# Optimization experiments

Hardware: AMD Instinct MI355X
Metric: run time of the kernel (lower is better)

## Reference

```python
import jax, jax.numpy as jnp
import numpy as np
import math

N, D, E, M, MODS = 16384, 1024, 5, 64, 5
K = 1  # top-k for sparse router


def setup_inputs() -> dict:
    key = jax.random.key(0)
    ks = jax.random.split(key, 24)
    rn = lambda k, shape, s=1.0: jax.random.normal(k, shape, dtype=jnp.float32) * s
    inp = {
        'x': rn(ks[0], (N, D)),
        'spectrogram': rn(ks[1], (N, D)),
        'waveform': rn(ks[2], (N, D)),
        'pitch': rn(ks[3], (N, D)),
        'envelope': rn(ks[4], (N, D)),
        'phase': rn(ks[5], (N, D)),
        # routers (torch Linear: y = x @ W.T + b, W is [out,in]); init std=0.01
        'Wsoft': rn(ks[6], (E, D), 0.01), 'bsoft': jnp.zeros((E,), jnp.float32),
        'Wsparse': rn(ks[7], (E, D), 0.01), 'bsparse': jnp.zeros((E,), jnp.float32),
        # memory (plain randn, not re-initialized)
        'm_key': rn(ks[8], (M, D)), 'm_val': rn(ks[9], (M, E)),
        # experts: Linear(D,D) -> SiLU -> Linear(D,D), stacked over E
        'W1': rn(ks[10], (E, D, D), 0.01), 'b1': jnp.zeros((E, D), jnp.float32),
        'W2': rn(ks[11], (E, D, D), 0.01), 'b2': jnp.zeros((E, D), jnp.float32),
        # fusion gates: Linear(D,1) + sigmoid, one per modality
        'Wg': rn(ks[12], (MODS, D), 0.01), 'bg': jnp.zeros((MODS,), jnp.float32),
        # fusion projection: Linear(D*MODS, D)
        'Wf': rn(ks[13], (D, D * MODS), 0.01), 'bf': jnp.zeros((D,), jnp.float32),
    }
    return inp


def reference(x, spectrogram, waveform, pitch, envelope, phase,
              Wsoft, bsoft, Wsparse, bsparse, m_key, m_val,
              W1, b1, W2, b2, Wg, bg, Wf, bf):
    alpha_moe = jnp.float32(0.5)
    alpha_fusion = jnp.float32(0.5)

    # soft router: softmax(Linear)
    soft_w = jax.nn.softmax(x @ Wsoft.T + bsoft, axis=-1)          # [N,E]

    # sparse router: top-k + softmax, scattered back to [N,E]
    logits = x @ Wsparse.T + bsparse                               # [N,E]
    top_vals, top_idx = jax.lax.top_k(logits, K)                   # [N,K]
    sparse_gates = jax.nn.softmax(top_vals, axis=-1)               # [N,K]
    one_hot = jax.nn.one_hot(top_idx, E, dtype=logits.dtype)       # [N,K,E]
    sparse_w = jnp.sum(one_hot * sparse_gates[..., None], axis=1)  # [N,E]

    # memory-augmented gating
    attn = jax.nn.softmax((x @ m_key.T) / math.sqrt(D), axis=-1)   # [N,M]
    memory_w = jax.nn.softmax(attn @ m_val, axis=-1)               # [N,E]

    mixed_w = alpha_moe * sparse_w + (1 - alpha_moe) * soft_w
    final_w = (mixed_w + memory_w) / 2                             # [N,E]

    # dense all-expert MLP: [N,E,D]
    h = jax.nn.silu(jnp.einsum('nd,eod->neo', x, W1) + b1)
    expert_out = jnp.einsum('ned,eod->neo', h, W2) + b2
    moe_output = jnp.einsum('neo,ne->no', expert_out, final_w)     # [N,D]

    # gated multimodal fusion
    features = [spectrogram, waveform, pitch, envelope, phase]
    gates = jax.nn.sigmoid(x @ Wg.T + bg)                          # [N,MODS]
    scaled = [gates[:, q:q + 1] * features[q] for q in range(MODS)]
    fused = jnp.concatenate(scaled, axis=-1) @ Wf.T + bf           # [N,D]

    return alpha_fusion * fused + (1 - alpha_fusion) * moe_output
```

## Files before the change

kernel.cpp:

```cpp
#include <hip/hip_runtime.h>
#include <stdint.h>

typedef __bf16 bf16x8 __attribute__((ext_vector_type(8)));
typedef float f32x4 __attribute__((ext_vector_type(4)));
typedef unsigned short u16;
typedef u16 ushort8 __attribute__((ext_vector_type(8)));

__device__ __forceinline__ u16 f2bf(float f) {
    uint32_t u = __builtin_bit_cast(uint32_t, f);
    u += 0x7FFFu + ((u >> 16) & 1u);
    return (u16)(u >> 16);
}

__device__ __forceinline__ void gload16(const void* g, void* l) {
    __builtin_amdgcn_global_load_lds(
        reinterpret_cast<const __attribute__((address_space(1))) void*>(reinterpret_cast<uintptr_t>(g)),
        reinterpret_cast<__attribute__((address_space(3))) void*>(reinterpret_cast<uintptr_t>(l)),
        16, 0, 0);
}

#define BAR() asm volatile("s_barrier" ::: "memory")

template <int MODE>
__global__ __launch_bounds__(512, 2)
void gemm256(const u16* __restrict__ A, int lda,
             const u16* __restrict__ B, int ldb, int K,
             void* __restrict__ Cout, int ldc,
             const float* __restrict__ bias, const float* __restrict__ fw05)
{
    __shared__ __align__(16) u16 As[2 * 256 * 64];
    __shared__ __align__(16) u16 Bs[2 * 256 * 64];

    const int t    = threadIdx.x;
    const int lane = t & 63;
    const int wave = t >> 6;
    const int l16  = lane & 15;
    const int lhi  = lane >> 4;
    const int wm   = wave >> 2;
    const int wn   = wave & 3;

    const size_t rowBase = (size_t)blockIdx.y * 256;
    const int    colBase = blockIdx.x * 256;
    const int    NT      = K >> 6;

    const int rl0 = t >> 3;
    const int ko0 = (t & 7) * 8;
    const int kos = ((t & 7) ^ (rl0 & 7)) * 8;

    const u16* aRow = A + (rowBase + rl0) * (size_t)lda + kos;
    const u16* bRow = B + (size_t)(colBase + rl0) * ldb + kos;
    u16* asW = As + rl0 * 64 + ko0;
    u16* bsW = Bs + rl0 * 64 + ko0;

#define STA(bufo, e, r0, r1)                                                     \
    do {                                                                         \
        gload16(aRow + (size_t)(r0) * lda + (e), asW + (bufo) + (r0) * 64);      \
        gload16(aRow + (size_t)(r1) * lda + (e), asW + (bufo) + (r1) * 64);      \
    } while (0)
#define STB(bufo, e, b0)                                                         \
    do {                                                                         \
        gload16(bRow + (size_t)(b0) * ldb + (e), bsW + (bufo) + (b0) * 64);      \
        gload16(bRow + (size_t)((b0) + 64) * ldb + (e),                          \
                bsW + (bufo) + ((b0) + 64) * 64);                                \
    } while (0)

    const int sw = l16 & 7;
    const u16* aRd0 = As + (wm * 128 + l16) * 64 + ((lhi ^ sw) * 8);
    const u16* aRd1 = As + (wm * 128 + l16) * 64 + (((lhi + 4) ^ sw) * 8);
    const u16* bRd0 = Bs + (wn * 64 + l16) * 64 + ((lhi ^ sw) * 8);
    const u16* bRd1 = Bs + (wn * 64 + l16) * 64 + (((lhi + 4) ^ sw) * 8);

    f32x4 acc[8][4];
#pragma unroll
    for (int i = 0; i < 8; i++)
#pragma unroll
        for (int j = 0; j < 4; j++)
            acc[i][j] = (f32x4){0.f, 0.f, 0.f, 0.f};

    STA(0, 0, 0, 128);
    STA(0, 0, 64, 192);
    STB(0, 0, 0);
    STB(0, 0, 128);
    const int e1p = (NT > 1) ? 64 : 0;
    STB(16384, e1p, 0);
    STB(16384, e1p, 128);
    STA(16384, e1p, 0, 128);
    asm volatile("s_waitcnt vmcnt(6)" ::: "memory");
    BAR();

    bf16x8 bfr[4][2];
    for (int tt = 0; tt < NT; ++tt) {
        const int c  = (tt & 1) << 14;
        const int cn = c ^ 16384;
        const int e1 = ((tt + 1 < NT) ? tt + 1 : NT - 1) << 6;
        const int e2 = ((tt + 2 < NT) ? tt + 2 : NT - 1) << 6;

#pragma unroll
        for (int q = 0; q < 4; ++q) {
            bf16x8 af[2][2];
#pragma unroll
            for (int s = 0; s < 2; ++s) {
                af[s][0] = *(const bf16x8*)(aRd0 + c + (2 * q + s) * 16 * 64);
                af[s][1] = *(const bf16x8*)(aRd1 + c + (2 * q + s) * 16 * 64);
            }
            if (q == 0) {
#pragma unroll
                for (int ni = 0; ni < 4; ++ni) {
                    bfr[ni][0] = *(const bf16x8*)(bRd0 + c + ni * 16 * 64);
                    bfr[ni][1] = *(const bf16x8*)(bRd1 + c + ni * 16 * 64);
                }
                STA(cn, e1, 64, 192);
            } else if (q == 1) {
                STB(c, e2, 0);
            } else if (q == 2) {
                STB(c, e2, 128);
            } else {
                STA(c, e2, 0, 128);
            }
            BAR();
            __builtin_amdgcn_s_setprio(1);
#pragma unroll
            for (int s = 0; s < 2; ++s)
#pragma unroll
                for (int ni = 0; ni < 4; ++ni)
#pragma unroll
                    for (int kk = 0; kk < 2; ++kk)
                        acc[2 * q + s][ni] = __builtin_amdgcn_mfma_f32_16x16x32_bf16(
                            af[s][kk], bfr[ni][kk], acc[2 * q + s][ni], 0, 0, 0);
            __builtin_amdgcn_s_setprio(0);
            if (q == 3) asm volatile("s_waitcnt vmcnt(6)" ::: "memory");
            BAR();
        }
    }

    const int orow = wm * 128 + lhi * 4;
    const int ocol = colBase + wn * 64 + l16;

    if constexpr (MODE == 0) {
        u16* C = (u16*)Cout;
#pragma unroll
        for (int mi = 0; mi < 8; mi++) {
#pragma unroll
            for (int j = 0; j < 4; j++) {
                size_t r = rowBase + orow + mi * 16 + j;
#pragma unroll
                for (int ni = 0; ni < 4; ni++) {
                    int cc = ocol + ni * 16;
                    float v = acc[mi][ni][j] + bias[cc];
                    float s = v / (1.f + __expf(-v));
                    C[r * (size_t)ldc + cc] = f2bf(fw05[r * 5 + (cc >> 10)] * s);
                }
            }
        }
    } else {
        float* C = (float*)Cout;
#pragma unroll
        for (int mi = 0; mi < 8; mi++) {
#pragma unroll
            for (int j = 0; j < 4; j++) {
                size_t r = rowBase + orow + mi * 16 + j;
#pragma unroll
                for (int ni = 0; ni < 4; ni++) {
                    size_t idx = r * (size_t)ldc + (ocol + ni * 16);
                    if constexpr (MODE == 1) C[idx] = acc[mi][ni][j];
                    else                     C[idx] += acc[mi][ni][j];
                }
            }
        }
    }
#undef STA
#undef STB
}

__global__ __launch_bounds__(256)
void router_kernel(const float* __restrict__ x,
                   const float* __restrict__ Wsoft, const float* __restrict__ Wsparse,
                   const float* __restrict__ m_key, const float* __restrict__ Wg,
                   float* __restrict__ logits)
{
    __shared__ float Xs[128][66];
    __shared__ float Ws[80][132];

    const int t    = threadIdx.x;
    const int lane = t & 63;
    const int wave = t >> 6;
    const int row0 = blockIdx.x * 64;

    float acc[20];
#pragma unroll
    for (int c = 0; c < 20; c++) acc[c] = 0.f;

    for (int k0 = 0; k0 < 1024; k0 += 128) {
#pragma unroll
        for (int i = 0; i < 8; i++) {
            int f4 = i * 256 + t;
            int r  = f4 >> 5;
            int kk = (f4 & 31) * 4;
            f32x4 v = *(const f32x4*)(x + (size_t)(row0 + r) * 1024 + k0 + kk);
            Xs[kk + 0][r] = v[0]; Xs[kk + 1][r] = v[1];
            Xs[kk + 2][r] = v[2]; Xs[kk + 3][r] = v[3];
        }
#pragma unroll
        for (int i = 0; i < 10; i++) {
            int f4 = i * 256 + t;
            int j  = f4 >> 5;
            int kk = (f4 & 31) * 4;
            const float* src;
            if      (j < 5)  src = Wsoft   + (size_t)j * 1024;
            else if (j < 10) src = Wsparse + (size_t)(j - 5) * 1024;
            else if (j < 74) src = m_key   + (size_t)(j - 10) * 1024;
            else             src = Wg      + (size_t)(j - 74) * 1024;
            *(f32x4*)&Ws[j][kk] = *(const f32x4*)(src + k0 + kk);
        }
        __syncthreads();

        for (int k4 = 0; k4 < 32; k4++) {
            float x0 = Xs[k4 * 4 + 0][lane];
            float x1 = Xs[k4 * 4 + 1][lane];
            float x2 = Xs[k4 * 4 + 2][lane];
            float x3 = Xs[k4 * 4 + 3][lane];
#pragma unroll
            for (int c = 0; c < 20; c++) {
                f32x4 w = *(const f32x4*)&Ws[wave * 20 + c][k4 * 4];
                acc[c] += x0 * w[0] + x1 * w[1] + x2 * w[2] + x3 * w[3];
            }
        }
        __syncthreads();
    }

    float* dst = logits + (size_t)(row0 + lane) * 80 + wave * 20;
#pragma unroll
    for (int c = 0; c < 20; c++) dst[c] = acc[c];
}

__global__ __launch_bounds__(256)
void finalize_kernel(const float* __restrict__ logits, const float* __restrict__ m_val,
                     const float* __restrict__ bsoft, const float* __restrict__ bsparse,
                     const float* __restrict__ bg,
                     float* __restrict__ fw05, float* __restrict__ g05, int NC)
{
    __shared__ float mv[320];
    for (int i = threadIdx.x; i < 320; i += 256) mv[i] = m_val[i];
    __syncthreads();

    int idx = blockIdx.x * 256 + threadIdx.x;
    if (idx >= NC) return;
    const float* L = logits + (size_t)idx * 80;

    float sl[5];
#pragma unroll
    for (int e = 0; e < 5; e++) sl[e] = L[e] + bsoft[e];
    float sm = sl[0];
#pragma unroll
    for (int e = 1; e < 5; e++) sm = fmaxf(sm, sl[e]);
    float ssum = 0.f, sw[5];
#pragma unroll
    for (int e = 0; e < 5; e++) { sw[e] = __expf(sl[e] - sm); ssum += sw[e]; }
    float sinv = 1.f / ssum;

    int am = 0; float bv = L[5] + bsparse[0];
#pragma unroll
    for (int e = 1; e < 5; e++) {
        float v = L[5 + e] + bsparse[e];
        if (v > bv) { bv = v; am = e; }
    }

    float amax = -1e30f;
    for (int m = 0; m < 64; m++) amax = fmaxf(amax, L[10 + m] * 0.03125f);
    float asum = 0.f, mw[5] = {0.f, 0.f, 0.f, 0.f, 0.f};
    for (int m = 0; m < 64; m++) {
        float a = __expf(L[10 + m] * 0.03125f - amax);
        asum += a;
#pragma unroll
        for (int e = 0; e < 5; e++) mw[e] += a * mv[m * 5 + e];
    }
    float ainv = 1.f / asum;
#pragma unroll
    for (int e = 0; e < 5; e++) mw[e] *= ainv;
    float mm = mw[0];
#pragma unroll
    for (int e = 1; e < 5; e++) mm = fmaxf(mm, mw[e]);
    float msum = 0.f, me[5];
#pragma unroll
    for (int e = 0; e < 5; e++) { me[e] = __expf(mw[e] - mm); msum += me[e]; }
    float minv = 1.f / msum;

#pragma unroll
    for (int e = 0; e < 5; e++)
        fw05[(size_t)idx * 5 + e] =
            0.125f * ((e == am) ? 1.f : 0.f) + 0.125f * sw[e] * sinv + 0.25f * me[e] * minv;
#pragma unroll
    for (int q = 0; q < 5; q++)
        g05[(size_t)idx * 5 + q] = 0.5f / (1.f + __expf(-(L[74 + q] + bg[q])));
}

__global__ __launch_bounds__(256)
void cast_bf16_kernel(const float* __restrict__ src, u16* __restrict__ dst, size_t n)
{
    size_t i = ((size_t)blockIdx.x * 256 + threadIdx.x) * 8;
    if (i >= n) return;
    f32x4 a = *(const f32x4*)(src + i);
    f32x4 b = *(const f32x4*)(src + i + 4);
    ushort8 o;
    o[0] = f2bf(a[0]); o[1] = f2bf(a[1]); o[2] = f2bf(a[2]); o[3] = f2bf(a[3]);
    o[4] = f2bf(b[0]); o[5] = f2bf(b[1]); o[6] = f2bf(b[2]); o[7] = f2bf(b[3]);
    *(ushort8*)(dst + i) = o;
}

__global__ __launch_bounds__(256)
void prep_w2cat(const float* __restrict__ W2, const float* __restrict__ b2,
                u16* __restrict__ out)
{
    size_t tid = (size_t)blockIdx.x * 256 + threadIdx.x;
    int o  = (int)(tid / 648);
    int c0 = (int)(tid % 648) * 8;
    ushort8 v;
    if (c0 + 8 <= 5120) {
        int e = c0 >> 10, d = c0 & 1023;
        const float* s = W2 + ((size_t)e * 1024 + o) * 1024 + d;
        f32x4 a = *(const f32x4*)s;
        f32x4 b = *(const f32x4*)(s + 4);
        v[0] = f2bf(a[0]); v[1] = f2bf(a[1]); v[2] = f2bf(a[2]); v[3] = f2bf(a[3]);
        v[4] = f2bf(b[0]); v[5] = f2bf(b[1]); v[6] = f2bf(b[2]); v[7] = f2bf(b[3]);
    } else {
#pragma unroll
        for (int jj = 0; jj < 8; jj++) {
            int c = c0 + jj;
            float f = (c >= 5120 && c < 5125) ? b2[(size_t)(c - 5120) * 1024 + o] : 0.f;
            v[jj] = f2bf(f);
        }
    }
    *(ushort8*)(out + (size_t)o * 5184 + c0) = v;
}

__global__ __launch_bounds__(256)
void prep_wfcat(const float* __restrict__ Wf, const float* __restrict__ bfias,
                u16* __restrict__ out)
{
    size_t tid = (size_t)blockIdx.x * 256 + threadIdx.x;
    int o  = (int)(tid / 648);
    int c0 = (int)(tid % 648) * 8;
    ushort8 v;
    if (c0 + 8 <= 5120) {
        const float* s = Wf + (size_t)o * 5120 + c0;
        f32x4 a = *(const f32x4*)s;
        f32x4 b = *(const f32x4*)(s + 4);
        v[0] = f2bf(a[0]); v[1] = f2bf(a[1]); v[2] = f2bf(a[2]); v[3] = f2bf(a[3]);
        v[4] = f2bf(b[0]); v[5] = f2bf(b[1]); v[6] = f2bf(b[2]); v[7] = f2bf(b[3]);
    } else {
#pragma unroll
        for (int jj = 0; jj < 8; jj++) {
            int c = c0 + jj;
            v[jj] = f2bf((c == 5120) ? bfias[o] : 0.f);
        }
    }
    *(ushort8*)(out + (size_t)o * 5184 + c0) = v;
}

__global__ __launch_bounds__(256)
void build_afused(const float* __restrict__ f0, const float* __restrict__ f1,
                  const float* __restrict__ f2, const float* __restrict__ f3,
                  const float* __restrict__ f4,
                  const float* __restrict__ g05, u16* __restrict__ Abuf)
{
    size_t tid = (size_t)blockIdx.x * 256 + threadIdx.x;
    size_t r  = tid / 640;
    int   c0  = (int)(tid % 640) * 8;
    int   q   = c0 >> 10;
    int   d   = c0 & 1023;
    const float* fq = (q == 0) ? f0 : (q == 1) ? f1 : (q == 2) ? f2 : (q == 3) ? f3 : f4;
    float g = g05[r * 5 + q];
    f32x4 a = *(const f32x4*)(fq + r * 1024 + d);
    f32x4 b = *(const f32x4*)(fq + r * 1024 + d + 4);
    ushort8 v;
    v[0] = f2bf(g * a[0]); v[1] = f2bf(g * a[1]); v[2] = f2bf(g * a[2]); v[3] = f2bf(g * a[3]);
    v[4] = f2bf(g * b[0]); v[5] = f2bf(g * b[1]); v[6] = f2bf(g * b[2]); v[7] = f2bf(g * b[3]);
    *(ushort8*)(Abuf + r * 5184 + c0) = v;
}

__global__ __launch_bounds__(256)
void fill_tail(const float* __restrict__ fw05, u16* __restrict__ Abuf, int NC, int mode)
{
    int r = blockIdx.x * 256 + threadIdx.x;
    if (r >= NC) return;
    u16* dst = Abuf + (size_t)r * 5184 + 5120;
    if (mode == 0) {
#pragma unroll
        for (int e = 0; e < 5; e++) dst[e] = f2bf(fw05[(size_t)r * 5 + e]);
        for (int j = 5; j < 64; j++) dst[j] = 0;
    } else {
        dst[0] = f2bf(0.5f);
        for (int j = 1; j < 64; j++) dst[j] = 0;
    }
}

extern "C" void kernel_launch(void* const* d_in, const int* in_sizes, int n_in,
                              void* d_out, int out_size, void* d_ws, size_t ws_size,
                              hipStream_t stream)
{
    (void)in_sizes; (void)n_in; (void)out_size;

    const float* x      = (const float*)d_in[0];
    const float* spect  = (const float*)d_in[1];
    const float* wavef  = (const float*)d_in[2];
    const float* pitch  = (const float*)d_in[3];
    const float* envel  = (const float*)d_in[4];
    const float* phase  = (const float*)d_in[5];
    const float* Wsoft  = (const float*)d_in[6];
    const float* bsoft  = (const float*)d_in[7];
    const float* Wsparse= (const float*)d_in[8];
    const float* bsparse= (const float*)d_in[9];
    const float* m_key  = (const float*)d_in[10];
    const float* m_val  = (const float*)d_in[11];
    const float* W1     = (const float*)d_in[12];
    const float* b1     = (const float*)d_in[13];
    const float* W2     = (const float*)d_in[14];
    const float* b2     = (const float*)d_in[15];
    const float* Wg     = (const float*)d_in[16];
    const float* bg     = (const float*)d_in[17];
    const float* Wf     = (const float*)d_in[18];
    const float* bfias  = (const float*)d_in[19];
    float* out = (float*)d_out;

    const int N = 16384;

    size_t fixed = (size_t)5 * 1024 * 1024 * 2 + 2 * (size_t)1024 * 5184 * 2;
    int NC = 16384;
    while (NC > 256 && fixed + (size_t)NC * 12776 > ws_size) NC >>= 1;

    char* p = (char*)d_ws;
    u16* W1bf  = (u16*)p; p += (size_t)5 * 1024 * 1024 * 2;
    u16* W2cat = (u16*)p; p += (size_t)1024 * 5184 * 2;
    u16* Wfcat = (u16*)p; p += (size_t)1024 * 5184 * 2;
    u16* Xbf   = (u16*)p; p += (size_t)NC * 1024 * 2;
    u16* Abuf  = (u16*)p; p += (size_t)NC * 5184 * 2;
    float* logits = (float*)p; p += (size_t)NC * 80 * 4;
    float* fw05   = (float*)p; p += (size_t)NC * 5 * 4;
    float* g05    = (float*)p; p += (size_t)NC * 5 * 4;

    cast_bf16_kernel<<<2560, 256, 0, stream>>>(W1, W1bf, (size_t)5 * 1024 * 1024);
    prep_w2cat<<<2592, 256, 0, stream>>>(W2, b2, W2cat);
    prep_wfcat<<<2592, 256, 0, stream>>>(Wf, bfias, Wfcat);

    for (int n0 = 0; n0 < N; n0 += NC) {
        const float* xc = x + (size_t)n0 * 1024;

        router_kernel<<<NC / 64, 256, 0, stream>>>(xc, Wsoft, Wsparse, m_key, Wg, logits);
        finalize_kernel<<<(NC + 255) / 256, 256, 0, stream>>>(logits, m_val, bsoft, bsparse, bg,
                                                              fw05, g05, NC);
        cast_bf16_kernel<<<NC / 2, 256, 0, stream>>>(xc, Xbf, (size_t)NC * 1024);

        gemm256<0><<<dim3(20, NC / 256), 512, 0, stream>>>(
            Xbf, 1024, W1bf, 1024, 1024, Abuf, 5184, b1, fw05);
        fill_tail<<<(NC + 255) / 256, 256, 0, stream>>>(fw05, Abuf, NC, 0);

        gemm256<1><<<dim3(4, NC / 256), 512, 0, stream>>>(
            Abuf, 5184, W2cat, 5184, 5184, out + (size_t)n0 * 1024, 1024, nullptr, nullptr);

        build_afused<<<(unsigned)((size_t)NC * 640 / 256), 256, 0, stream>>>(
            spect + (size_t)n0 * 1024, wavef + (size_t)n0 * 1024,
            pitch + (size_t)n0 * 1024, envel + (size_t)n0 * 1024,
            phase + (size_t)n0 * 1024, g05, Abuf);
        fill_tail<<<(NC + 255) / 256, 256, 0, stream>>>(fw05, Abuf, NC, 1);

        gemm256<2><<<dim3(4, NC / 256), 512, 0, stream>>>(
            Abuf, 5184, Wfcat, 5184, 5184, out + (size_t)n0 * 1024, 1024, nullptr, nullptr);
    }
}
```

Measured before the change: 747.0 us.

## Merge MoE and fusion GEMMs into one K-concatenated GEMM, fuse prep kernels

Concatenates the expert-down GEMM and the fusion-projection GEMM along K into a single GEMM of K=10368 that writes the output directly, removing the read-modify-write second pass. The gated feature scaling is folded into the first GEMM's epilogue, the x bf16 cast into the router kernel, and the bias/tail columns into finalize, so build_afused, fill_tail and cast kernels are gone. It also adds a grouped block-index swizzle for L2 locality. The cost is a larger activation buffer (possibly smaller chunks on a tight workspace) and a heavier, less balanced GEMM epilogue in the first GEMM.

```diff
diff --git a/kernel.cpp b/kernel.cpp
--- a/kernel.cpp
+++ b/kernel.cpp
@@ -5,6 +5,7 @@
 typedef float f32x4 __attribute__((ext_vector_type(4)));
 typedef unsigned short u16;
 typedef u16 ushort8 __attribute__((ext_vector_type(8)));
+typedef u16 ushort4v __attribute__((ext_vector_type(4)));
 
 __device__ __forceinline__ u16 f2bf(float f) {
     uint32_t u = __builtin_bit_cast(uint32_t, f);
@@ -26,7 +27,11 @@
 void gemm256(const u16* __restrict__ A, int lda,
              const u16* __restrict__ B, int ldb, int K,
              void* __restrict__ Cout, int ldc,
-             const float* __restrict__ bias, const float* __restrict__ fw05)
+             const float* __restrict__ bias, const float* __restrict__ fw05,
+             const float* __restrict__ g05,
+             const float* __restrict__ f0, const float* __restrict__ f1,
+             const float* __restrict__ f2, const float* __restrict__ f3,
+             const float* __restrict__ f4)
 {
     __shared__ __align__(16) u16 As[2 * 256 * 64];
     __shared__ __align__(16) u16 Bs[2 * 256 * 64];
@@ -39,8 +44,15 @@
     const int wm   = wave >> 2;
     const int wn   = wave & 3;
 
-    const size_t rowBase = (size_t)blockIdx.y * 256;
-    const int    colBase = blockIdx.x * 256;
+    const int gx  = gridDim.x;
+    const int nwg = gx * gridDim.y;
+    int id  = blockIdx.y * gx + blockIdx.x;
+    int swz = (nwg & 7) ? id : ((id & 7) * (nwg >> 3) + (id >> 3));
+    const int bx = swz % gx;
+    const int by = swz / gx;
+
+    const size_t rowBase = (size_t)by * 256;
+    const int    colBase = bx * 256;
     const int    NT      = K >> 6;
 
     const int rl0 = t >> 3;
@@ -138,18 +150,42 @@
 
     if constexpr (MODE == 0) {
         u16* C = (u16*)Cout;
+        const int eidx = colBase >> 10;
 #pragma unroll
         for (int mi = 0; mi < 8; mi++) {
 #pragma unroll
             for (int j = 0; j < 4; j++) {
                 size_t r = rowBase + orow + mi * 16 + j;
+                float w = fw05[r * 5 + eidx];
 #pragma unroll
                 for (int ni = 0; ni < 4; ni++) {
                     int cc = ocol + ni * 16;
                     float v = acc[mi][ni][j] + bias[cc];
                     float s = v / (1.f + __expf(-v));
-                    C[r * (size_t)ldc + cc] = f2bf(fw05[r * 5 + (cc >> 10)] * s);
+                    C[r * (size_t)ldc + cc] = f2bf(w * s);
                 }
+            }
+        }
+        {
+            const float* fq = (eidx == 0) ? f0 : (eidx == 1) ? f1
+                             : (eidx == 2) ? f2 : (eidx == 3) ? f3 : f4;
+            const int dbase = colBase & 1023;
+            const int r2  = t >> 1;
+            const int cb0 = (t & 1) * 128;
+            const size_t r = rowBase + r2;
+            const float g = g05[r * 5 + eidx];
+            const float* fr = fq + r * 1024 + dbase + cb0;
+            u16* dst = C + r * (size_t)ldc + 5184 + colBase + cb0;
+#pragma unroll
+            for (int i = 0; i < 16; ++i) {
+                f32x4 a = *(const f32x4*)(fr + i * 8);
+                f32x4 b = *(const f32x4*)(fr + i * 8 + 4);
+                ushort8 v;
+                v[0] = f2bf(g * a[0]); v[1] = f2bf(g * a[1]);
+                v[2] = f2bf(g * a[2]); v[3] = f2bf(g * a[3]);
+                v[4] = f2bf(g * b[0]); v[5] = f2bf(g * b[1]);
+                v[6] = f2bf(g * b[2]); v[7] = f2bf(g * b[3]);
+                *(ushort8*)(dst + i * 8) = v;
             }
         }
     } else {
@@ -162,8 +198,7 @@
 #pragma unroll
                 for (int ni = 0; ni < 4; ni++) {
                     size_t idx = r * (size_t)ldc + (ocol + ni * 16);
-                    if constexpr (MODE == 1) C[idx] = acc[mi][ni][j];
-                    else                     C[idx] += acc[mi][ni][j];
+                    C[idx] = acc[mi][ni][j];
                 }
             }
         }
@@ -176,7 +211,7 @@
 void router_kernel(const float* __restrict__ x,
                    const float* __restrict__ Wsoft, const float* __restrict__ Wsparse,
                    const float* __restrict__ m_key, const float* __restrict__ Wg,
-                   float* __restrict__ logits)
+                   float* __restrict__ logits, u16* __restrict__ Xbf)
 {
     __shared__ float Xs[128][66];
     __shared__ float Ws[80][132];
@@ -199,6 +234,10 @@
             f32x4 v = *(const f32x4*)(x + (size_t)(row0 + r) * 1024 + k0 + kk);
             Xs[kk + 0][r] = v[0]; Xs[kk + 1][r] = v[1];
             Xs[kk + 2][r] = v[2]; Xs[kk + 3][r] = v[3];
+            ushort4v o4;
+            o4[0] = f2bf(v[0]); o4[1] = f2bf(v[1]);
+            o4[2] = f2bf(v[2]); o4[3] = f2bf(v[3]);
+            *(ushort4v*)(Xbf + (size_t)(row0 + r) * 1024 + k0 + kk) = o4;
         }
 #pragma unroll
         for (int i = 0; i < 10; i++) {
@@ -237,7 +276,8 @@
 void finalize_kernel(const float* __restrict__ logits, const float* __restrict__ m_val,
                      const float* __restrict__ bsoft, const float* __restrict__ bsparse,
                      const float* __restrict__ bg,
-                     float* __restrict__ fw05, float* __restrict__ g05, int NC)
+                     float* __restrict__ fw05, float* __restrict__ g05,
+                     u16* __restrict__ Abuf, int NC)
 {
     __shared__ float mv[320];
     for (int i = threadIdx.x; i < 320; i += 256) mv[i] = m_val[i];
@@ -285,13 +325,21 @@
     for (int e = 0; e < 5; e++) { me[e] = __expf(mw[e] - mm); msum += me[e]; }
     float minv = 1.f / msum;
 
-#pragma unroll
-    for (int e = 0; e < 5; e++)
-        fw05[(size_t)idx * 5 + e] =
-            0.125f * ((e == am) ? 1.f : 0.f) + 0.125f * sw[e] * sinv + 0.25f * me[e] * minv;
+    u16* ta = Abuf + (size_t)idx * 10368;
+#pragma unroll
+    for (int e = 0; e < 5; e++) {
+        float fv = 0.125f * ((e == am) ? 1.f : 0.f) + 0.125f * sw[e] * sinv
+                 + 0.25f * me[e] * minv;
+        fw05[(size_t)idx * 5 + e] = fv;
+        ta[5120 + e] = f2bf(fv);
+    }
 #pragma unroll
     for (int q = 0; q < 5; q++)
         g05[(size_t)idx * 5 + q] = 0.5f / (1.f + __expf(-(L[74 + q] + bg[q])));
+
+    for (int j = 5125; j < 5184; j++) ta[j] = 0;
+    ta[10304] = f2bf(0.5f);
+    for (int j = 10305; j < 10368; j++) ta[j] = 0;
 }
 
 __global__ __launch_bounds__(256)
@@ -308,12 +356,13 @@
 }
 
 __global__ __launch_bounds__(256)
-void prep_w2cat(const float* __restrict__ W2, const float* __restrict__ b2,
-                u16* __restrict__ out)
+void prep_wcat(const float* __restrict__ W2, const float* __restrict__ b2,
+               const float* __restrict__ Wf, const float* __restrict__ bfias,
+               u16* __restrict__ out)
 {
     size_t tid = (size_t)blockIdx.x * 256 + threadIdx.x;
-    int o  = (int)(tid / 648);
-    int c0 = (int)(tid % 648) * 8;
+    int o  = (int)(tid / 1296);
+    int c0 = (int)(tid % 1296) * 8;
     ushort8 v;
     if (c0 + 8 <= 5120) {
         int e = c0 >> 10, d = c0 & 1023;
@@ -322,76 +371,30 @@
         f32x4 b = *(const f32x4*)(s + 4);
         v[0] = f2bf(a[0]); v[1] = f2bf(a[1]); v[2] = f2bf(a[2]); v[3] = f2bf(a[3]);
         v[4] = f2bf(b[0]); v[5] = f2bf(b[1]); v[6] = f2bf(b[2]); v[7] = f2bf(b[3]);
-    } else {
+    } else if (c0 < 5184) {
 #pragma unroll
         for (int jj = 0; jj < 8; jj++) {
             int c = c0 + jj;
             float f = (c >= 5120 && c < 5125) ? b2[(size_t)(c - 5120) * 1024 + o] : 0.f;
             v[jj] = f2bf(f);
         }
-    }
-    *(ushort8*)(out + (size_t)o * 5184 + c0) = v;
-}
-
-__global__ __launch_bounds__(256)
-void prep_wfcat(const float* __restrict__ Wf, const float* __restrict__ bfias,
-                u16* __restrict__ out)
-{
-    size_t tid = (size_t)blockIdx.x * 256 + threadIdx.x;
-    int o  = (int)(tid / 648);
-    int c0 = (int)(tid % 648) * 8;
-    ushort8 v;
-    if (c0 + 8 <= 5120) {
-        const float* s = Wf + (size_t)o * 5120 + c0;
-        f32x4 a = *(const f32x4*)s;
-        f32x4 b = *(const f32x4*)(s + 4);
-        v[0] = f2bf(a[0]); v[1] = f2bf(a[1]); v[2] = f2bf(a[2]); v[3] = f2bf(a[3]);
-        v[4] = f2bf(b[0]); v[5] = f2bf(b[1]); v[6] = f2bf(b[2]); v[7] = f2bf(b[3]);
     } else {
-#pragma unroll
-        for (int jj = 0; jj < 8; jj++) {
-            int c = c0 + jj;
-            v[jj] = f2bf((c == 5120) ? bfias[o] : 0.f);
-        }
-    }
-    *(ushort8*)(out + (size_t)o * 5184 + c0) = v;
-}
-
-__global__ __launch_bounds__(256)
-void build_afused(const float* __restrict__ f0, const float* __restrict__ f1,
-                  const float* __restrict__ f2, const float* __restrict__ f3,
-                  const float* __restrict__ f4,
-                  const float* __restrict__ g05, u16* __restrict__ Abuf)
-{
-    size_t tid = (size_t)blockIdx.x * 256 + threadIdx.x;
-    size_t r  = tid / 640;
-    int   c0  = (int)(tid % 640) * 8;
-    int   q   = c0 >> 10;
-    int   d   = c0 & 1023;
-    const float* fq = (q == 0) ? f0 : (q == 1) ? f1 : (q == 2) ? f2 : (q == 3) ? f3 : f4;
-    float g = g05[r * 5 + q];
-    f32x4 a = *(const f32x4*)(fq + r * 1024 + d);
-    f32x4 b = *(const f32x4*)(fq + r * 1024 + d + 4);
-    ushort8 v;
-    v[0] = f2bf(g * a[0]); v[1] = f2bf(g * a[1]); v[2] = f2bf(g * a[2]); v[3] = f2bf(g * a[3]);
-    v[4] = f2bf(g * b[0]); v[5] = f2bf(g * b[1]); v[6] = f2bf(g * b[2]); v[7] = f2bf(g * b[3]);
-    *(ushort8*)(Abuf + r * 5184 + c0) = v;
-}
-
-__global__ __launch_bounds__(256)
-void fill_tail(const float* __restrict__ fw05, u16* __restrict__ Abuf, int NC, int mode)
-{
-    int r = blockIdx.x * 256 + threadIdx.x;
-    if (r >= NC) return;
-    u16* dst = Abuf + (size_t)r * 5184 + 5120;
-    if (mode == 0) {
-#pragma unroll
-        for (int e = 0; e < 5; e++) dst[e] = f2bf(fw05[(size_t)r * 5 + e]);
-        for (int j = 5; j < 64; j++) dst[j] = 0;
-    } else {
-        dst[0] = f2bf(0.5f);
-        for (int j = 1; j < 64; j++) dst[j] = 0;
-    }
+        int c2 = c0 - 5184;
+        if (c2 + 8 <= 5120) {
+            const float* s = Wf + (size_t)o * 5120 + c2;
+            f32x4 a = *(const f32x4*)s;
+            f32x4 b = *(const f32x4*)(s + 4);
+            v[0] = f2bf(a[0]); v[1] = f2bf(a[1]); v[2] = f2bf(a[2]); v[3] = f2bf(a[3]);
+            v[4] = f2bf(b[0]); v[5] = f2bf(b[1]); v[6] = f2bf(b[2]); v[7] = f2bf(b[3]);
+        } else {
+#pragma unroll
+            for (int jj = 0; jj < 8; jj++) {
+                int cj = c2 + jj;
+                v[jj] = f2bf((cj == 5120) ? bfias[o] : 0.f);
+            }
+        }
+    }
+    *(ushort8*)(out + (size_t)o * 10368 + c0) = v;
 }
 
 extern "C" void kernel_launch(void* const* d_in, const int* in_sizes, int n_in,
@@ -424,46 +427,36 @@
 
     const int N = 16384;
 
-    size_t fixed = (size_t)5 * 1024 * 1024 * 2 + 2 * (size_t)1024 * 5184 * 2;
+    size_t fixed = (size_t)5 * 1024 * 1024 * 2 + (size_t)1024 * 10368 * 2;
     int NC = 16384;
-    while (NC > 256 && fixed + (size_t)NC * 12776 > ws_size) NC >>= 1;
+    while (NC > 256 && fixed + (size_t)NC * 23144 > ws_size) NC >>= 1;
 
     char* p = (char*)d_ws;
-    u16* W1bf  = (u16*)p; p += (size_t)5 * 1024 * 1024 * 2;
-    u16* W2cat = (u16*)p; p += (size_t)1024 * 5184 * 2;
-    u16* Wfcat = (u16*)p; p += (size_t)1024 * 5184 * 2;
-    u16* Xbf   = (u16*)p; p += (size_t)NC * 1024 * 2;
-    u16* Abuf  = (u16*)p; p += (size_t)NC * 5184 * 2;
+    u16* W1bf = (u16*)p; p += (size_t)5 * 1024 * 1024 * 2;
+    u16* Wcat = (u16*)p; p += (size_t)1024 * 10368 * 2;
+    u16* Xbf  = (u16*)p; p += (size_t)NC * 1024 * 2;
+    u16* Abuf = (u16*)p; p += (size_t)NC * 10368 * 2;
     float* logits = (float*)p; p += (size_t)NC * 80 * 4;
     float* fw05   = (float*)p; p += (size_t)NC * 5 * 4;
     float* g05    = (float*)p; p += (size_t)NC * 5 * 4;
 
     cast_bf16_kernel<<<2560, 256, 0, stream>>>(W1, W1bf, (size_t)5 * 1024 * 1024);
-    prep_w2cat<<<2592, 256, 0, stream>>>(W2, b2, W2cat);
-    prep_wfcat<<<2592, 256, 0, stream>>>(Wf, bfias, Wfcat);
+    prep_wcat<<<5184, 256, 0, stream>>>(W2, b2, Wf, bfias, Wcat);
 
     for (int n0 = 0; n0 < N; n0 += NC) {
-        const float* xc = x + (size_t)n0 * 1024;
-
-        router_kernel<<<NC / 64, 256, 0, stream>>>(xc, Wsoft, Wsparse, m_key, Wg, logits);
-        finalize_kernel<<<(NC + 255) / 256, 256, 0, stream>>>(logits, m_val, bsoft, bsparse, bg,
-                                                              fw05, g05, NC);
-        cast_bf16_kernel<<<NC / 2, 256, 0, stream>>>(xc, Xbf, (size_t)NC * 1024);
+        const size_t off = (size_t)n0 * 1024;
+
+        router_kernel<<<NC / 64, 256, 0, stream>>>(x + off, Wsoft, Wsparse, m_key, Wg,
+                                                   logits, Xbf);
+        finalize_kernel<<<(NC + 255) / 256, 256, 0, stream>>>(
+            logits, m_val, bsoft, bsparse, bg, fw05, g05, Abuf, NC);
 
         gemm256<0><<<dim3(20, NC / 256), 512, 0, stream>>>(
-            Xbf, 1024, W1bf, 1024, 1024, Abuf, 5184, b1, fw05);
-        fill_tail<<<(NC + 255) / 256, 256, 0, stream>>>(fw05, Abuf, NC, 0);
+            Xbf, 1024, W1bf, 1024, 1024, Abuf, 10368, b1, fw05, g05,
+            spect + off, wavef + off, pitch + off, envel + off, phase + off);
 
         gemm256<1><<<dim3(4, NC / 256), 512, 0, stream>>>(
-            Abuf, 5184, W2cat, 5184, 5184, out + (size_t)n0 * 1024, 1024, nullptr, nullptr);
-
-        build_afused<<<(unsigned)((size_t)NC * 640 / 256), 256, 0, stream>>>(
-            spect + (size_t)n0 * 1024, wavef + (size_t)n0 * 1024,
-            pitch + (size_t)n0 * 1024, envel + (size_t)n0 * 1024,
-            phase + (size_t)n0 * 1024, g05, Abuf);
-        fill_tail<<<(NC + 255) / 256, 256, 0, stream>>>(fw05, Abuf, NC, 1);
-
-        gemm256<2><<<dim3(4, NC / 256), 512, 0, stream>>>(
-            Abuf, 5184, Wfcat, 5184, 5184, out + (size_t)n0 * 1024, 1024, nullptr, nullptr);
-    }
-}
+            Abuf, 10368, Wcat, 10368, 10368, out + off, 1024,
+            nullptr, nullptr, nullptr, nullptr, nullptr, nullptr, nullptr, nullptr);
+    }
+}
```

New measurement: 751.9 us. No clear change (+0.7%).
